# Performance work log

Hardware: AMD Instinct MI355X
Metric: run time of the kernel (lower is better)

The kernel has to match this reference:

```python
import jax, jax.numpy as jnp
import numpy as np

N_HEAD = 16

def setup_inputs() -> dict:
    key = jax.random.key(0)
    k1, k2, k3 = jax.random.split(key, 3)
    B, T, C = 2, 2048, 1024
    x = jax.random.normal(k1, (B, T, C), dtype=jnp.float32)
    W_attn = jax.random.normal(k2, (C, 3 * C), dtype=jnp.float32) * (C ** -0.5)
    b_attn = jnp.zeros((3 * C,), dtype=jnp.float32)
    W_proj = jax.random.normal(k3, (C, C), dtype=jnp.float32) * (C ** -0.5)
    b_proj = jnp.zeros((C,), dtype=jnp.float32)
    return {"x": x, "W_attn": W_attn, "b_attn": b_attn, "W_proj": W_proj, "b_proj": b_proj}

def reference(x, W_attn, b_attn, W_proj, b_proj):
    B, T, C = x.shape
    H = N_HEAD
    D = C // H  # head_dim
    scale = D ** -0.5
    qkv = x @ W_attn + b_attn                       # [B,T,3C]
    q, k, v = jnp.split(qkv, 3, axis=-1)
    # [B,T,C] -> [B,H,T,D]
    q = q.reshape(B, T, H, D).transpose(0, 2, 1, 3)
    k = k.reshape(B, T, H, D).transpose(0, 2, 1, 3)
    v = v.reshape(B, T, H, D).transpose(0, 2, 1, 3)
    att = jnp.einsum('bhqd,bhkd->bhqk', q, k) * scale
    causal = jnp.tril(jnp.ones((T, T), dtype=bool))
    att = jnp.where(causal, att, jnp.float32(-jnp.inf))
    att = jax.nn.softmax(att, axis=-1)
    y = jnp.einsum('bhqk,bhkd->bhqd', att, v)       # [B,H,T,D]
    y = y.transpose(0, 2, 1, 3).reshape(B, T, C)
    return y @ W_proj + b_proj
```

## Files before the change

kernel.cpp:

```cpp
#include <hip/hip_runtime.h>

typedef __bf16 bf16;
typedef __bf16 bf16x4 __attribute__((ext_vector_type(4)));
typedef __bf16 bf16x8 __attribute__((ext_vector_type(8)));
typedef short s16x4 __attribute__((ext_vector_type(4)));
typedef float f32x4 __attribute__((ext_vector_type(4)));
typedef unsigned int u32x4 __attribute__((ext_vector_type(4)));

#define NB 2
#define NT 2048
#define NC 1024
#define NH 16
#define ND 64

#if __has_builtin(__builtin_amdgcn_exp2f)
#define EXP2F(x) __builtin_amdgcn_exp2f(x)
#else
#define EXP2F(x) __expf(0.69314718055994531f * (x))
#endif

#if __has_builtin(__builtin_amdgcn_rcpf)
#define RCPF(x) __builtin_amdgcn_rcpf(x)
#else
#define RCPF(x) (1.0f / (x))
#endif

__device__ __forceinline__ void async16(const void* g, void* l) {
  __builtin_amdgcn_global_load_lds(
      (const __attribute__((address_space(1))) void*)g,
      (__attribute__((address_space(3))) void*)l, 16, 0, 0);
}

__device__ __forceinline__ bf16x8 ld8(const bf16* p) {
  return *reinterpret_cast<const bf16x8*>(p);
}
__device__ __forceinline__ bf16x4 ld4(const bf16* p) {
  return *reinterpret_cast<const bf16x4*>(p);
}

__device__ __forceinline__ f32x4 mfma16(bf16x4 a, bf16x4 b, f32x4 c) {
  s16x4 ai = __builtin_bit_cast(s16x4, a);
  s16x4 bi = __builtin_bit_cast(s16x4, b);
#if __has_builtin(__builtin_amdgcn_mfma_f32_16x16x16bf16_1k)
  return __builtin_amdgcn_mfma_f32_16x16x16bf16_1k(ai, bi, c, 0, 0, 0);
#else
  f32x4 d;
  asm("v_mfma_f32_16x16x16_bf16 %0, %1, %2, %3"
      : "=v"(d) : "v"(ai), "v"(bi), "v"(c));
  return d;
#endif
}

__global__ __launch_bounds__(256) void cvt_bf16(const float* __restrict__ src,
                                                bf16* __restrict__ dst, int n) {
  int i = (blockIdx.x * 256 + threadIdx.x) * 8;
  if (i + 8 <= n) {
    const float4* s = (const float4*)(src + i);
    float4 a = s[0], b = s[1];
    bf16x8 o;
    o[0] = (bf16)a.x; o[1] = (bf16)a.y; o[2] = (bf16)a.z; o[3] = (bf16)a.w;
    o[4] = (bf16)b.x; o[5] = (bf16)b.y; o[6] = (bf16)b.z; o[7] = (bf16)b.w;
    *(bf16x8*)(dst + i) = o;
  }
}

__global__ __launch_bounds__(256) void transpose_cvt(const float* __restrict__ src,
                                                     bf16* __restrict__ dst,
                                                     int R, int Cc) {
  __shared__ float tile[32][33];
  int tx = threadIdx.x & 31, ty = threadIdx.x >> 5;
  int r0 = blockIdx.y * 32, c0 = blockIdx.x * 32;
#pragma unroll
  for (int i = 0; i < 4; ++i)
    tile[ty + i * 8][tx] = src[(size_t)(r0 + ty + i * 8) * Cc + c0 + tx];
  __syncthreads();
#pragma unroll
  for (int i = 0; i < 4; ++i)
    dst[(size_t)(c0 + ty + i * 8) * R + r0 + tx] = (bf16)tile[tx][ty + i * 8];
}

__global__ __launch_bounds__(256) void transpose_v(const bf16* __restrict__ V,
                                                   bf16* __restrict__ Vt) {
  __shared__ bf16 t[64][72];
  const int tid = threadIdx.x;
  const int bh = blockIdx.y;
  const int t0 = blockIdx.x * 64;
  const int r = tid >> 2, c = (tid & 3) * 16;
  const bf16* src = V + ((size_t)bh * NT + t0 + r) * ND + c;
  bf16x8 a = ld8(src), b = ld8(src + 8);
#pragma unroll
  for (int j = 0; j < 8; ++j) { t[c + j][r] = a[j]; t[c + 8 + j][r] = b[j]; }
  __syncthreads();
  bf16* dst = Vt + ((size_t)bh * ND + r) * NT + t0 + c;
  *(bf16x8*)dst = ld8(&t[r][c]);
  *(bf16x8*)(dst + 8) = ld8(&t[r][c + 8]);
}

__global__ __launch_bounds__(256, 2) void gemm_qkv(
    const bf16* __restrict__ A,
    const bf16* __restrict__ Bt,
    const float* __restrict__ bias,
    bf16* __restrict__ Qo, bf16* __restrict__ Ko, bf16* __restrict__ Vo) {
  const int K = 1024;
  __shared__ bf16 As[128 * 32];
  __shared__ bf16 Bs[128 * 32];
  const int tid = threadIdx.x;
  const int lane = tid & 63, wv = tid >> 6;
  const int quad = lane >> 4, ln = lane & 15;
  const int m0 = blockIdx.x * 128, n0 = blockIdx.y * 128;
  const int wr = (wv >> 1) * 64, wc = (wv & 1) * 64;
  const int rA = tid >> 2, cA = (tid & 3) * 8;
  f32x4 acc[4][4] = {};

  for (int kt = 0; kt < K / 32; ++kt) {
    const int k0 = kt * 32;
#pragma unroll
    for (int inst = 0; inst < 2; ++inst) {
      async16(A + (size_t)(m0 + inst * 64 + rA) * K + k0 + cA,
              &As[inst * 2048 + wv * 512]);
      async16(Bt + (size_t)(n0 + inst * 64 + rA) * K + k0 + cA,
              &Bs[inst * 2048 + wv * 512]);
    }
    __syncthreads();
    bf16x8 aF[4], bF[4];
#pragma unroll
    for (int i = 0; i < 4; ++i) {
      aF[i] = ld8(&As[(wr + i * 16 + ln) * 32 + quad * 8]);
      bF[i] = ld8(&Bs[(wc + i * 16 + ln) * 32 + quad * 8]);
    }
#pragma unroll
    for (int rb = 0; rb < 4; ++rb)
#pragma unroll
      for (int cb = 0; cb < 4; ++cb)
        acc[rb][cb] = __builtin_amdgcn_mfma_f32_16x16x32_bf16(
            aF[rb], bF[cb], acc[rb][cb], 0, 0, 0);
    __syncthreads();
  }
#pragma unroll
  for (int rb = 0; rb < 4; ++rb) {
#pragma unroll
    for (int cb = 0; cb < 4; ++cb) {
      int gn = n0 + wc + cb * 16 + ln;
      int part = gn >> 10, c = gn & 1023;
      int h = c >> 6, dd = c & 63;
      float bs = bias[gn];
      bf16* dst = part == 0 ? Qo : (part == 1 ? Ko : Vo);
      float sc = part == 0 ? 0.18033688f : 1.0f;
#pragma unroll
      for (int r = 0; r < 4; ++r) {
        int gm = m0 + wr + rb * 16 + quad * 4 + r;
        int b = gm >> 11, t = gm & 2047;
        dst[((size_t)(b * NH + h) * NT + t) * ND + dd] =
            (bf16)((acc[rb][cb][r] + bs) * sc);
      }
    }
  }
}

__global__ __launch_bounds__(256, 2) void flash_attn_kernel(
    const bf16* __restrict__ Qg, const bf16* __restrict__ Kg,
    const bf16* __restrict__ Vtg, bf16* __restrict__ Yg) {
  __shared__ __align__(16) char smem[2][16384];
  const int tid = threadIdx.x;
  const int lane = tid & 63, wv = tid >> 6;
  const int quad = lane >> 4, ln = lane & 15;
  const int bid = blockIdx.x;
  const int qt = 15 - (bid >> 5);
  const int bh = bid & 31;
  const int bb = bh >> 4, hh = bh & 15;
  const int q0 = qt * 128;
  const int q0w = q0 + wv * 32;
  const bf16* Qp = Qg + ((size_t)bh * NT + q0w) * ND;
  const bf16* Kbase = Kg + (size_t)bh * NT * ND;
  const bf16* Vtbase = Vtg + (size_t)bh * ND * NT;

  const int sub = lane >> 3, sch = lane & 7;

  bf16x8 qf[2][2];
#pragma unroll
  for (int rb = 0; rb < 2; ++rb)
#pragma unroll
    for (int ks = 0; ks < 2; ++ks)
      qf[rb][ks] = ld8(Qp + (size_t)(rb * 16 + ln) * ND + ks * 32 + quad * 8);

  f32x4 oacc[2][4] = {};
  float mi[2] = {-1e30f, -1e30f}, li[2] = {0.f, 0.f};

  const int ktiles = 2 * qt + 2;
  const int cw = 2 * qt + 1 + (wv >> 1);
  const int swz = ln & 7;

#define STAGE(KT, P)                                                           \
  {                                                                            \
    const int k0s = (KT) * 64;                                                 \
    char* Kl = smem[P];                                                        \
    char* Vl = smem[P] + 8192;                                                 \
    _Pragma("unroll") for (int i = 0; i < 2; ++i) {                            \
      int r0 = wv * 16 + i * 8;                                                \
      int row = r0 + sub;                                                      \
      int gch = sch ^ (row & 7);                                               \
      async16(Kbase + (size_t)(k0s + row) * ND + gch * 8, Kl + r0 * 128);      \
      async16(Vtbase + (size_t)row * NT + k0s + gch * 8, Vl + r0 * 128);       \
    }                                                                          \
  }

  STAGE(0, 0);
  for (int kt = 0; kt < ktiles; ++kt) {
    const int p = kt & 1;
    __syncthreads();
    if (kt + 1 < ktiles) STAGE(kt + 1, p ^ 1);
    if (kt < cw) {
      const char* Kl = smem[p];
      const char* Vl = smem[p] + 8192;
      const int k0 = kt * 64;
      f32x4 sacc[2][4] = {};
#pragma unroll
      for (int ks = 0; ks < 2; ++ks) {
        bf16x8 kfr[4];
#pragma unroll
        for (int cb = 0; cb < 4; ++cb)
          kfr[cb] = *(const bf16x8*)(Kl + (cb * 16 + ln) * 128 +
                                     (((ks * 4 + quad) ^ swz) * 16));
#pragma unroll
        for (int rb = 0; rb < 2; ++rb)
#pragma unroll
          for (int cb = 0; cb < 4; ++cb)
            sacc[rb][cb] = __builtin_amdgcn_mfma_f32_16x16x32_bf16(
                kfr[cb], qf[rb][ks], sacc[rb][cb], 0, 0, 0);
      }
      if (k0 + 63 > q0w) {
#pragma unroll
        for (int rb = 0; rb < 2; ++rb) {
          int qr = q0w + rb * 16 + ln;
#pragma unroll
          for (int cb = 0; cb < 4; ++cb)
#pragma unroll
            for (int r = 0; r < 4; ++r) {
              int kc = k0 + cb * 16 + quad * 4 + r;
              if (kc > qr) sacc[rb][cb][r] = -1e30f;
            }
        }
      }
      bf16x4 pf[2][4];
      float alpha[2];
#pragma unroll
      for (int rb = 0; rb < 2; ++rb) {
        float mx = -1e30f;
#pragma unroll
        for (int cb = 0; cb < 4; ++cb)
#pragma unroll
          for (int r = 0; r < 4; ++r) mx = fmaxf(mx, sacc[rb][cb][r]);
        mx = fmaxf(mx, __shfl_xor(mx, 16));
        mx = fmaxf(mx, __shfl_xor(mx, 32));
        float mnew = fmaxf(mi[rb], mx);
        alpha[rb] = EXP2F(mi[rb] - mnew);
        mi[rb] = mnew;
        float rs = 0.f;
#pragma unroll
        for (int cb = 0; cb < 4; ++cb) {
          bf16x4 pv;
#pragma unroll
          for (int r = 0; r < 4; ++r) {
            float pexp = EXP2F(sacc[rb][cb][r] - mnew);
            rs += pexp;
            pv[r] = (bf16)pexp;
          }
          pf[rb][cb] = pv;
        }
        rs += __shfl_xor(rs, 16);
        rs += __shfl_xor(rs, 32);
        li[rb] = li[rb] * alpha[rb] + rs;
      }
#pragma unroll
      for (int rb = 0; rb < 2; ++rb)
#pragma unroll
        for (int db = 0; db < 4; ++db)
#pragma unroll
          for (int r = 0; r < 4; ++r) oacc[rb][db][r] *= alpha[rb];
#pragma unroll
      for (int cb = 0; cb < 4; ++cb) {
        bf16x4 vfr[4];
#pragma unroll
        for (int db = 0; db < 4; ++db)
          vfr[db] = *(const bf16x4*)(Vl + (db * 16 + ln) * 128 +
                                     (((cb * 2 + (quad >> 1)) ^ swz) * 16) +
                                     (quad & 1) * 8);
#pragma unroll
        for (int rb = 0; rb < 2; ++rb)
#pragma unroll
          for (int db = 0; db < 4; ++db)
            oacc[rb][db] = mfma16(vfr[db], pf[rb][cb], oacc[rb][db]);
      }
    }
  }
#undef STAGE

#pragma unroll
  for (int rb = 0; rb < 2; ++rb) {
    float inv = RCPF(li[rb]);
    int row = q0w + rb * 16 + ln;
#pragma unroll
    for (int db = 0; db < 4; ++db) {
      bf16x4 ov;
#pragma unroll
      for (int r = 0; r < 4; ++r) ov[r] = (bf16)(oacc[rb][db][r] * inv);
      *(bf16x4*)(Yg + ((size_t)(bb * NT + row)) * NC + hh * 64 + db * 16 +
                 quad * 4) = ov;
    }
  }
}

__global__ __launch_bounds__(256, 2) void gemm_proj(
    const bf16* __restrict__ A,
    const bf16* __restrict__ Bt,
    const float* __restrict__ bias,
    float* __restrict__ out) {
  const int K = 1024;
  __shared__ bf16 As[128 * 32];
  __shared__ bf16 Bs[128 * 32];
  const int tid = threadIdx.x;
  const int lane = tid & 63, wv = tid >> 6;
  const int quad = lane >> 4, ln = lane & 15;
  const int m0 = blockIdx.x * 128, n0 = blockIdx.y * 128;
  const int wr = (wv >> 1) * 64, wc = (wv & 1) * 64;
  const int rA = tid >> 2, cA = (tid & 3) * 8;
  f32x4 acc[4][4] = {};

  for (int kt = 0; kt < K / 32; ++kt) {
    const int k0 = kt * 32;
#pragma unroll
    for (int inst = 0; inst < 2; ++inst) {
      async16(A + (size_t)(m0 + inst * 64 + rA) * K + k0 + cA,
              &As[inst * 2048 + wv * 512]);
      async16(Bt + (size_t)(n0 + inst * 64 + rA) * K + k0 + cA,
              &Bs[inst * 2048 + wv * 512]);
    }
    __syncthreads();
    bf16x8 aF[4], bF[4];
#pragma unroll
    for (int i = 0; i < 4; ++i) {
      aF[i] = ld8(&As[(wr + i * 16 + ln) * 32 + quad * 8]);
      bF[i] = ld8(&Bs[(wc + i * 16 + ln) * 32 + quad * 8]);
    }
#pragma unroll
    for (int rb = 0; rb < 4; ++rb)
#pragma unroll
      for (int cb = 0; cb < 4; ++cb)
        acc[rb][cb] = __builtin_amdgcn_mfma_f32_16x16x32_bf16(
            aF[rb], bF[cb], acc[rb][cb], 0, 0, 0);
    __syncthreads();
  }
#pragma unroll
  for (int rb = 0; rb < 4; ++rb) {
#pragma unroll
    for (int cb = 0; cb < 4; ++cb) {
      int gn = n0 + wc + cb * 16 + ln;
      float bs = bias[gn];
#pragma unroll
      for (int r = 0; r < 4; ++r) {
        int gm = m0 + wr + rb * 16 + quad * 4 + r;
        out[(size_t)gm * 1024 + gn] = acc[rb][cb][r] + bs;
      }
    }
  }
}

extern "C" void kernel_launch(void* const* d_in, const int* in_sizes, int n_in,
                              void* d_out, int out_size, void* d_ws, size_t ws_size,
                              hipStream_t stream) {
  const float* x      = (const float*)d_in[0];
  const float* W_attn = (const float*)d_in[1];
  const float* b_attn = (const float*)d_in[2];
  const float* W_proj = (const float*)d_in[3];
  const float* b_proj = (const float*)d_in[4];
  float* out = (float*)d_out;

  bf16* ws  = (bf16*)d_ws;
  bf16* xb  = ws;
  bf16* Wab = xb + (size_t)4096 * 1024;
  bf16* Wpb = Wab + (size_t)3072 * 1024;
  bf16* Qb  = Wpb + (size_t)1024 * 1024;
  bf16* Kb  = Qb + (size_t)32 * 2048 * 64;
  bf16* Vb  = Kb + (size_t)32 * 2048 * 64;
  bf16* Vtb = xb;
  bf16* Yb  = Vb;

  cvt_bf16<<<2048, 256, 0, stream>>>(x, xb, 4096 * 1024);
  transpose_cvt<<<dim3(96, 32), 256, 0, stream>>>(W_attn, Wab, 1024, 3072);
  transpose_cvt<<<dim3(32, 32), 256, 0, stream>>>(W_proj, Wpb, 1024, 1024);
  gemm_qkv<<<dim3(32, 24), 256, 0, stream>>>(xb, Wab, b_attn, Qb, Kb, Vb);
  transpose_v<<<dim3(32, 32), 256, 0, stream>>>(Vb, Vtb);
  flash_attn_kernel<<<512, 256, 0, stream>>>(Qb, Kb, Vtb, Yb);
  gemm_proj<<<dim3(32, 8), 256, 0, stream>>>(Yb, Wpb, b_proj, out);
}
```

Before: 190.0 us.

## Fuse V transpose into QKV GEMM, merge weight transposes, shrink attention blocks

The QKV GEMM epilogue now writes V directly in transposed [bh, D, T] layout using 4-element vector stores, which removes the separate transpose_v kernel and its extra pass over V. The two weight transpose-convert launches are merged into one kernel that picks its source by block index. The flash attention kernel moves to 64-query tiles with 128 threads and 1024 blocks, so each block loads a full 64-row K/V tile per stage and the per-wave causal skip is dropped. The aim is fewer launches and better load balance across the causal triangle. The cost is more K/V reloading per query and strided stores into Vt.

```diff
diff --git a/kernel.cpp b/kernel.cpp
--- a/kernel.cpp
+++ b/kernel.cpp
@@ -64,43 +64,32 @@
   }
 }
 
-__global__ __launch_bounds__(256) void transpose_cvt(const float* __restrict__ src,
-                                                     bf16* __restrict__ dst,
-                                                     int R, int Cc) {
+__global__ __launch_bounds__(256) void transpose_cvt2(
+    const float* __restrict__ Wa, bf16* __restrict__ Da,
+    const float* __restrict__ Wp, bf16* __restrict__ Dp) {
   __shared__ float tile[32][33];
+  int bx = blockIdx.x;
+  const float* src;
+  bf16* dst;
+  int Cc;
+  if (bx < 96) { src = Wa; dst = Da; Cc = 3072; }
+  else         { src = Wp; dst = Dp; Cc = 1024; bx -= 96; }
   int tx = threadIdx.x & 31, ty = threadIdx.x >> 5;
-  int r0 = blockIdx.y * 32, c0 = blockIdx.x * 32;
+  int r0 = blockIdx.y * 32, c0 = bx * 32;
 #pragma unroll
   for (int i = 0; i < 4; ++i)
     tile[ty + i * 8][tx] = src[(size_t)(r0 + ty + i * 8) * Cc + c0 + tx];
   __syncthreads();
 #pragma unroll
   for (int i = 0; i < 4; ++i)
-    dst[(size_t)(c0 + ty + i * 8) * R + r0 + tx] = (bf16)tile[tx][ty + i * 8];
-}
-
-__global__ __launch_bounds__(256) void transpose_v(const bf16* __restrict__ V,
-                                                   bf16* __restrict__ Vt) {
-  __shared__ bf16 t[64][72];
-  const int tid = threadIdx.x;
-  const int bh = blockIdx.y;
-  const int t0 = blockIdx.x * 64;
-  const int r = tid >> 2, c = (tid & 3) * 16;
-  const bf16* src = V + ((size_t)bh * NT + t0 + r) * ND + c;
-  bf16x8 a = ld8(src), b = ld8(src + 8);
-#pragma unroll
-  for (int j = 0; j < 8; ++j) { t[c + j][r] = a[j]; t[c + 8 + j][r] = b[j]; }
-  __syncthreads();
-  bf16* dst = Vt + ((size_t)bh * ND + r) * NT + t0 + c;
-  *(bf16x8*)dst = ld8(&t[r][c]);
-  *(bf16x8*)(dst + 8) = ld8(&t[r][c + 8]);
+    dst[(size_t)(c0 + ty + i * 8) * 1024 + r0 + tx] = (bf16)tile[tx][ty + i * 8];
 }
 
 __global__ __launch_bounds__(256, 2) void gemm_qkv(
     const bf16* __restrict__ A,
     const bf16* __restrict__ Bt,
     const float* __restrict__ bias,
-    bf16* __restrict__ Qo, bf16* __restrict__ Ko, bf16* __restrict__ Vo) {
+    bf16* __restrict__ Qo, bf16* __restrict__ Ko, bf16* __restrict__ Vto) {
   const int K = 1024;
   __shared__ bf16 As[128 * 32];
   __shared__ bf16 Bs[128 * 32];
@@ -144,20 +133,26 @@
       int part = gn >> 10, c = gn & 1023;
       int h = c >> 6, dd = c & 63;
       float bs = bias[gn];
-      bf16* dst = part == 0 ? Qo : (part == 1 ? Ko : Vo);
-      float sc = part == 0 ? 0.18033688f : 1.0f;
-#pragma unroll
-      for (int r = 0; r < 4; ++r) {
-        int gm = m0 + wr + rb * 16 + quad * 4 + r;
-        int b = gm >> 11, t = gm & 2047;
-        dst[((size_t)(b * NH + h) * NT + t) * ND + dd] =
-            (bf16)((acc[rb][cb][r] + bs) * sc);
-      }
-    }
-  }
-}
-
-__global__ __launch_bounds__(256, 2) void flash_attn_kernel(
+      int gm0 = m0 + wr + rb * 16 + quad * 4;
+      int b = gm0 >> 11, t0 = gm0 & 2047;
+      if (part == 2) {
+        bf16x4 vv;
+#pragma unroll
+        for (int r = 0; r < 4; ++r) vv[r] = (bf16)(acc[rb][cb][r] + bs);
+        *(bf16x4*)(Vto + ((size_t)(b * NH + h) * ND + dd) * NT + t0) = vv;
+      } else {
+        bf16* dst = part == 0 ? Qo : Ko;
+        float sc = part == 0 ? 0.18033688f : 1.0f;
+#pragma unroll
+        for (int r = 0; r < 4; ++r)
+          dst[((size_t)(b * NH + h) * NT + t0 + r) * ND + dd] =
+              (bf16)((acc[rb][cb][r] + bs) * sc);
+      }
+    }
+  }
+}
+
+__global__ __launch_bounds__(128, 2) void flash_attn_kernel(
     const bf16* __restrict__ Qg, const bf16* __restrict__ Kg,
     const bf16* __restrict__ Vtg, bf16* __restrict__ Yg) {
   __shared__ __align__(16) char smem[2][16384];
@@ -165,16 +160,16 @@
   const int lane = tid & 63, wv = tid >> 6;
   const int quad = lane >> 4, ln = lane & 15;
   const int bid = blockIdx.x;
-  const int qt = 15 - (bid >> 5);
+  const int qt = 31 - (bid >> 5);
   const int bh = bid & 31;
   const int bb = bh >> 4, hh = bh & 15;
-  const int q0 = qt * 128;
-  const int q0w = q0 + wv * 32;
+  const int q0w = qt * 64 + wv * 32;
   const bf16* Qp = Qg + ((size_t)bh * NT + q0w) * ND;
   const bf16* Kbase = Kg + (size_t)bh * NT * ND;
   const bf16* Vtbase = Vtg + (size_t)bh * ND * NT;
 
   const int sub = lane >> 3, sch = lane & 7;
+  const int swz = ln & 7;
 
   bf16x8 qf[2][2];
 #pragma unroll
@@ -186,17 +181,15 @@
   f32x4 oacc[2][4] = {};
   float mi[2] = {-1e30f, -1e30f}, li[2] = {0.f, 0.f};
 
-  const int ktiles = 2 * qt + 2;
-  const int cw = 2 * qt + 1 + (wv >> 1);
-  const int swz = ln & 7;
+  const int ktiles = qt + 1;
 
 #define STAGE(KT, P)                                                           \
   {                                                                            \
     const int k0s = (KT) * 64;                                                 \
     char* Kl = smem[P];                                                        \
     char* Vl = smem[P] + 8192;                                                 \
-    _Pragma("unroll") for (int i = 0; i < 2; ++i) {                            \
-      int r0 = wv * 16 + i * 8;                                                \
+    _Pragma("unroll") for (int i = 0; i < 4; ++i) {                            \
+      int r0 = wv * 32 + i * 8;                                                \
       int row = r0 + sub;                                                      \
       int gch = sch ^ (row & 7);                                               \
       async16(Kbase + (size_t)(k0s + row) * ND + gch * 8, Kl + r0 * 128);      \
@@ -209,7 +202,7 @@
     const int p = kt & 1;
     __syncthreads();
     if (kt + 1 < ktiles) STAGE(kt + 1, p ^ 1);
-    if (kt < cw) {
+    {
       const char* Kl = smem[p];
       const char* Vl = smem[p] + 8192;
       const int k0 = kt * 64;
@@ -381,15 +374,12 @@
   bf16* Wpb = Wab + (size_t)3072 * 1024;
   bf16* Qb  = Wpb + (size_t)1024 * 1024;
   bf16* Kb  = Qb + (size_t)32 * 2048 * 64;
-  bf16* Vb  = Kb + (size_t)32 * 2048 * 64;
-  bf16* Vtb = xb;
-  bf16* Yb  = Vb;
+  bf16* Vtb = Kb + (size_t)32 * 2048 * 64;
+  bf16* Yb  = xb;
 
   cvt_bf16<<<2048, 256, 0, stream>>>(x, xb, 4096 * 1024);
-  transpose_cvt<<<dim3(96, 32), 256, 0, stream>>>(W_attn, Wab, 1024, 3072);
-  transpose_cvt<<<dim3(32, 32), 256, 0, stream>>>(W_proj, Wpb, 1024, 1024);
-  gemm_qkv<<<dim3(32, 24), 256, 0, stream>>>(xb, Wab, b_attn, Qb, Kb, Vb);
-  transpose_v<<<dim3(32, 32), 256, 0, stream>>>(Vb, Vtb);
-  flash_attn_kernel<<<512, 256, 0, stream>>>(Qb, Kb, Vtb, Yb);
+  transpose_cvt2<<<dim3(128, 32), 256, 0, stream>>>(W_attn, Wab, W_proj, Wpb);
+  gemm_qkv<<<dim3(32, 24), 256, 0, stream>>>(xb, Wab, b_attn, Qb, Kb, Vtb);
+  flash_attn_kernel<<<1024, 128, 0, stream>>>(Qb, Kb, Vtb, Yb);
   gemm_proj<<<dim3(32, 8), 256, 0, stream>>>(Yb, Wpb, b_proj, out);
 }
```

Result: no change. 188.3 us (-0.9%).
